# Kernel optimization log

Measured on AMD Instinct MI355X. Metric: run time of the kernel, lower is better.

## Reference

```python
import jax, jax.numpy as jnp
import numpy as np

B, T, HU, C = 256, 128, 512, 64

def setup_inputs() -> dict:
    key = jax.random.key(0)
    k = jax.random.split(key, 8)
    H = jax.random.normal(k[0], (B, T, HU), dtype=jnp.float32)
    y = jax.random.randint(k[1], (B, T), 0, C)
    y_len = jax.random.randint(k[2], (B,), 1, T + 1).astype(jnp.int32)
    y_mask = (jnp.arange(T)[None, :] < y_len[:, None]).astype(jnp.float32)
    xav = float(np.sqrt(6.0 / (3 * HU + C)))
    W = jax.random.uniform(k[3], (C, 3 * HU), minval=-xav, maxval=xav, dtype=jnp.float32)
    b = jnp.zeros((C,), dtype=jnp.float32)
    start_transitions = jax.random.uniform(k[4], (C,), minval=-1.0, maxval=1.0, dtype=jnp.float32)
    end_transitions = jax.random.uniform(k[5], (C,), minval=-1.0, maxval=1.0, dtype=jnp.float32)
    transitions = jax.random.uniform(k[6], (C, C), minval=-1.0, maxval=1.0, dtype=jnp.float32)
    return {"H": H, "W": W, "b": b, "start_transitions": start_transitions,
            "end_transitions": end_transitions, "transitions": transitions,
            "y": y, "y_mask": y_mask, "y_len": y_len}

def _crf_ll(H, W, b, start_transitions, end_transitions, transitions, y, y_mask, y_len):
    Bn, Tn, hu = H.shape
    zeros = jnp.zeros((Bn, 1, hu), H.dtype)
    prev = jnp.concatenate([zeros, H[:, :-1, :]], axis=1)
    nxt = jnp.concatenate([H[:, 1:, :], zeros], axis=1)
    context = jnp.concatenate([prev, H, nxt], axis=-1)            # [B,T,3h]
    scores = jnp.einsum('bth,ch->btc', context, W) + b            # [B,T,C]

    # numerator (gold path score)
    em_sel = jnp.take_along_axis(scores, y[..., None], axis=2)[..., 0]  # [B,T]
    num = start_transitions[y[:, 0]]
    num = num + jnp.sum(em_sel[:, :-1] * y_mask[:, :-1], axis=1)
    num = num + jnp.sum(transitions[y[:, :-1], y[:, 1:]] * y_mask[:, 1:], axis=1)
    last_tags = jnp.take_along_axis(y, (y_len - 1)[:, None].astype(y.dtype), axis=1)[:, 0]
    num = num + end_transitions[last_tags]
    num = num + jnp.take_along_axis(scores[:, -1, :], last_tags[:, None], axis=1)[:, 0] * y_mask[:, -1]

    # partition (log Z) via masked logsumexp scan
    em_t = jnp.transpose(scores, (1, 0, 2))   # [T,B,C]
    m_t = y_mask.T                            # [T,B]
    lp0 = start_transitions[None, :] + em_t[0]
    def step(lp, inp):
        em, m = inp
        new = jax.nn.logsumexp(lp[:, :, None] + transitions[None, :, :] + em[:, None, :], axis=1)
        lp = new * m[:, None] + lp * (1.0 - m[:, None])
        return lp, None
    lp, _ = jax.lax.scan(step, lp0, (em_t[1:], m_t[1:]))
    logZ = jax.nn.logsumexp(lp + end_transitions[None, :], axis=1)
    return num - logZ                          # [B]

def reference(H, W, b, start_transitions, end_transitions, transitions, y, y_mask, y_len):
    return _crf_ll(H, W, b, start_transitions, end_transitions, transitions, y, y_mask, y_len)
```

## Files before the change

kernel.cpp:

```cpp
#include <hip/hip_runtime.h>

typedef __attribute__((ext_vector_type(8))) short short8;
typedef __attribute__((ext_vector_type(4))) float f32x4;

__device__ __forceinline__ unsigned pk_rne(float a, float b) {
  unsigned short ha = __builtin_bit_cast(unsigned short, (_Float16)a);
  unsigned short hb = __builtin_bit_cast(unsigned short, (_Float16)b);
  return (unsigned)ha | ((unsigned)hb << 16);
}
__device__ __forceinline__ unsigned short f2bf(float x) {
  unsigned int u = __float_as_uint(x);
  u += 0x7FFFu + ((u >> 16) & 1u);
  return (unsigned short)(u >> 16);
}
__device__ __forceinline__ float bf2f(unsigned short h) {
  return __uint_as_float(((unsigned)h) << 16);
}
__device__ __forceinline__ unsigned pk_bf(float a, float b) {
  unsigned r;
  asm("v_cvt_pk_bf16_f32 %0, %1, %2" : "=v"(r) : "v"(a), "v"(b));
  return r;
}
__device__ __forceinline__ unsigned scale_bf_pair(unsigned w, float s) {
  float f0 = __uint_as_float(w << 16) * s;
  float f1 = __uint_as_float(w & 0xFFFF0000u) * s;
  return pk_bf(f0, f1);
}

__global__ __launch_bounds__(512) void crf_fused_kernel(
    const float* __restrict__ H, const float* __restrict__ W,
    const float* __restrict__ bias,
    const float* __restrict__ startT, const float* __restrict__ endT,
    const float* __restrict__ trans,
    const int* __restrict__ y, const int* __restrict__ y_len,
    float* __restrict__ out)
{
  __shared__ __align__(16) float smem[25088];
  __shared__ __align__(16) unsigned char EAbuf[8192];
  __shared__ __align__(16) float sc[128][68];
  __shared__ float scm[128];
  __shared__ float emy[128];
  __shared__ __align__(16) float ubuf[64];
  unsigned char* aTh = (unsigned char*)smem;
  unsigned char* bTh = aTh + 16384;
  float* P = smem;
  unsigned char* Mbase = (unsigned char*)smem;

  const int b    = blockIdx.x;
  const int tid  = threadIdx.x;
  const int lane = tid & 63;
  const int wid  = tid >> 6;
  const int wm   = wid >> 2;
  const int wn   = wid & 3;

  f32x4 acc[4][3] = {};
  const float* Hb = H + (size_t)b * (128 * 512);
  const int len = y_len[b];
  const int* yb = y + b * 128;

  float4 areg[4], breg[6];
  int aRow[4], aK4[4], bN[6], bK4[6];
  #pragma unroll
  for (int it = 0; it < 4; ++it) { int i = it * 512 + tid; aRow[it] = i >> 4; aK4[it] = i & 15; }
  #pragma unroll
  for (int it = 0; it < 6; ++it) { int i = it * 512 + tid; bN[it] = i >> 4; bK4[it] = i & 15; }
  #pragma unroll
  for (int it = 0; it < 4; ++it)
    areg[it] = ((const float4*)(Hb + aRow[it] * 512))[aK4[it]];
  #pragma unroll
  for (int it = 0; it < 6; ++it)
    breg[it] = ((const float4*)(W + (bN[it] & 63) * 1536 + (bN[it] >> 6) * 512))[bK4[it]];

  #pragma unroll
  for (int it = 0; it < 2; ++it) {
    int idx = it * 512 + tid;
    int c = idx >> 4, c4 = idx & 15;
    float4 v = ((const float4*)trans)[idx];
    #pragma unroll
    for (int e = 0; e < 4; ++e) {
      int cp = c4 * 4 + e;
      float val = __expf(((const float*)&v)[e] - 1.0f);
      *(unsigned short*)(EAbuf + cp * 128 + ((2 * c) ^ ((cp & 7) << 4))) = f2bf(val);
    }
  }

  for (int kk = 0; kk < 512; kk += 64) {
    if (kk) __syncthreads();
    #pragma unroll
    for (int it = 0; it < 4; ++it) {
      float4 v = areg[it];
      uint2 hi; hi.x = pk_rne(v.x, v.y); hi.y = pk_rne(v.z, v.w);
      int off = aRow[it] * 128 + ((aK4[it] * 8) ^ ((aRow[it] & 7) << 4));
      *(uint2*)(aTh + off) = hi;
    }
    #pragma unroll
    for (int it = 0; it < 6; ++it) {
      float4 v = breg[it];
      uint2 bh; bh.x = pk_rne(v.x, v.y); bh.y = pk_rne(v.z, v.w);
      int off = bN[it] * 128 + ((bK4[it] * 8) ^ ((bN[it] & 7) << 4));
      *(uint2*)(bTh + off) = bh;
    }
    __syncthreads();
    if (kk < 448) {
      #pragma unroll
      for (int it = 0; it < 4; ++it)
        areg[it] = ((const float4*)(Hb + aRow[it] * 512 + kk + 64))[aK4[it]];
      #pragma unroll
      for (int it = 0; it < 6; ++it)
        breg[it] = ((const float4*)(W + (bN[it] & 63) * 1536 + (bN[it] >> 6) * 512 + kk + 64))[bK4[it]];
    }
    #pragma unroll
    for (int ks = 0; ks < 2; ++ks) {
      const int kbyte = ks * 64 + ((lane >> 4) << 4);
      short8 ah[4], bh[3];
      #pragma unroll
      for (int m = 0; m < 4; ++m) {
        int row = wm * 64 + m * 16 + (lane & 15);
        ah[m] = *(const short8*)(aTh + row * 128 + (kbyte ^ ((row & 7) << 4)));
      }
      #pragma unroll
      for (int n = 0; n < 3; ++n) {
        int col = wn * 48 + n * 16 + (lane & 15);
        bh[n] = *(const short8*)(bTh + col * 128 + (kbyte ^ ((col & 7) << 4)));
      }
      #pragma unroll
      for (int m = 0; m < 4; ++m)
        #pragma unroll
        for (int n = 0; n < 3; ++n)
          asm("v_mfma_f32_16x16x32_f16 %0, %1, %2, %0"
              : "+v"(acc[m][n]) : "v"(ah[m]), "v"(bh[n]));
    }
  }
  __syncthreads();

  #pragma unroll
  for (int m = 0; m < 4; ++m)
    #pragma unroll
    for (int n = 0; n < 3; ++n) {
      int row0 = wm * 64 + m * 16 + ((lane >> 4) << 2);
      int col  = wn * 48 + n * 16 + (lane & 15);
      #pragma unroll
      for (int j = 0; j < 4; ++j)
        P[(row0 + j) * 196 + col] = acc[m][n][j];
    }
  __syncthreads();

  #pragma unroll
  for (int it = 0; it < 4; ++it) {
    int i4 = it * 512 + tid;
    int t = i4 >> 4, c4 = i4 & 15;
    float4 s = *(const float4*)(P + t * 196 + 64 + c4 * 4);
    float4 bb = ((const float4*)bias)[c4];
    s.x += bb.x; s.y += bb.y; s.z += bb.z; s.w += bb.w;
    if (t > 0) {
      float4 g = *(const float4*)(P + (t - 1) * 196 + c4 * 4);
      s.x += g.x; s.y += g.y; s.z += g.z; s.w += g.w;
    }
    if (t < 127) {
      float4 g = *(const float4*)(P + (t + 1) * 196 + 128 + c4 * 4);
      s.x += g.x; s.y += g.y; s.z += g.z; s.w += g.w;
    }
    *(float4*)(&sc[t][c4 * 4]) = s;
    float m4 = fmaxf(fmaxf(s.x, s.y), fmaxf(s.z, s.w));
    #pragma unroll
    for (int o = 1; o < 16; o <<= 1) m4 = fmaxf(m4, __shfl_xor(m4, o, 64));
    if ((lane & 15) == 0) scm[t] = m4;
    int yt = yb[t];
    if ((yt >> 2) == c4) {
      int r = yt & 3;
      emy[t] = (r == 0) ? s.x : (r == 1) ? s.y : (r == 2) ? s.z : s.w;
    }
  }
  __syncthreads();

  {
    int row = tid >> 2, c0 = (tid & 3) << 4;
    float mt = scm[row];
    float4* p4 = (float4*)&sc[row][c0];
    #pragma unroll
    for (int j = 0; j < 4; ++j) {
      float4 x = p4[j];
      x.x = __expf(x.x - mt); x.y = __expf(x.y - mt);
      x.z = __expf(x.z - mt); x.w = __expf(x.w - mt);
      p4[j] = x;
    }
  }
  float num = 0.f;
  if (wid == 0) {
    float p = 0.f;
    #pragma unroll
    for (int rep = 0; rep < 2; ++rep) {
      int t = lane + rep * 64;
      if (t < 127) {
        int yt = yb[t], yt1 = yb[t + 1];
        if (t < len)     p += emy[t];
        if (t + 1 < len) p += trans[yt * 64 + yt1];
      }
    }
    #pragma unroll
    for (int s = 32; s > 0; s >>= 1) p += __shfl_xor(p, s, 64);
    num = p + startT[yb[0]] + endT[yb[len - 1]];
    if (len == 128) num += emy[127];
  }
  __syncthreads();

  {
    unsigned char* Mb = Mbase + wid * 8192;
    int t0 = (wid == 0) ? 1 : 16 * wid;
    int t1 = 16 * wid + 15; if (t1 > len - 1) t1 = len - 1;
    if (t0 <= t1) {
      const int sw = (lane & 7) << 4;
      float s0 = sc[t0][lane];
      #pragma unroll
      for (int j = 0; j < 8; ++j) {
        uint4 w = *(const uint4*)(EAbuf + lane * 128 + ((j * 16) ^ sw));
        uint4 o;
        o.x = scale_bf_pair(w.x, s0); o.y = scale_bf_pair(w.y, s0);
        o.z = scale_bf_pair(w.z, s0); o.w = scale_bf_pair(w.w, s0);
        *(uint4*)(Mb + lane * 128 + ((j * 16) ^ sw)) = o;
      }
      short8 ea[4][2];
      #pragma unroll
      for (int rt = 0; rt < 4; ++rt)
        #pragma unroll
        for (int kh = 0; kh < 2; ++kh) {
          int row = rt * 16 + (lane & 15);
          int kb = kh * 64 + ((lane >> 4) << 4);
          ea[rt][kh] = *(const short8*)(EAbuf + row * 128 + (kb ^ ((row & 7) << 4)));
        }
      f32x4 z4 = {0.f, 0.f, 0.f, 0.f};
      for (int t = t0 + 1; t <= t1; ++t) {
        short8 mf[4][2];
        #pragma unroll
        for (int ct = 0; ct < 4; ++ct)
          #pragma unroll
          for (int kh = 0; kh < 2; ++kh) {
            int row = ct * 16 + (lane & 15);
            int kb = kh * 64 + ((lane >> 4) << 4);
            mf[ct][kh] = *(const short8*)(Mb + row * 128 + (kb ^ ((row & 7) << 4)));
          }
        f32x4 sv[4];
        #pragma unroll
        for (int rt = 0; rt < 4; ++rt)
          sv[rt] = *(const f32x4*)(&sc[t][rt * 16 + ((lane >> 4) << 2)]);
        f32x4 c[4][4];
        #pragma unroll
        for (int rt = 0; rt < 4; ++rt)
          #pragma unroll
          for (int ct = 0; ct < 4; ++ct) {
            asm("v_mfma_f32_16x16x32_bf16 %0, %1, %2, %3"
                : "=&v"(c[rt][ct]) : "v"(ea[rt][0]), "v"(mf[ct][0]), "v"(z4));
            asm("v_mfma_f32_16x16x32_bf16 %0, %1, %2, %0"
                : "+v"(c[rt][ct]) : "v"(ea[rt][1]), "v"(mf[ct][1]));
          }
        #pragma unroll
        for (int rt = 0; rt < 4; ++rt)
          #pragma unroll
          for (int ct = 0; ct < 4; ++ct) {
            f32x4 cc = c[rt][ct] * sv[rt];
            uint2 w2; w2.x = pk_bf(cc[0], cc[1]); w2.y = pk_bf(cc[2], cc[3]);
            int row = ct * 16 + (lane & 15);
            int byt = 2 * (rt * 16 + ((lane >> 4) << 2));
            *(uint2*)(Mb + row * 128 + (byt ^ ((row & 7) << 4))) = w2;
          }
      }
    }
  }
  __syncthreads();
  if (wid != 0) return;

  float eE = __expf(endT[lane]);
  float ls;
  {
    int t1 = 1 + lane, t2 = 65 + lane;
    float a = (t1 <= len - 1) ? (scm[t1] + 1.0f) : 0.f;
    if (t2 <= len - 1) a += scm[t2] + 1.0f;
    #pragma unroll
    for (int s = 32; s > 0; s >>= 1) a += __shfl_xor(a, s, 64);
    ls = a + scm[0];
  }
  float u = __expf(startT[lane]) * sc[0][lane];

  for (int k = 0; k < 8; ++k) {
    if (k && 16 * k >= len) break;
    int lo = (k == 0) ? 1 : 16 * k;
    int hi = 16 * k + 15; if (hi > len - 1) hi = len - 1;
    if (lo > hi) continue;
    float r = u;
    #pragma unroll
    for (int s = 32; s > 0; s >>= 1) r = fmaxf(r, __shfl_xor(r, s, 64));
    unsigned br = __float_as_uint(r) & 0x7F800000u;
    u *= __uint_as_float(0x7F000000u - br);
    ls += (float)((int)(br >> 23) - 127) * 0.69314718055994531f;
    const unsigned char* Mb = Mbase + k * 8192;
    ubuf[lane] = u;
    float v0 = 0.f, v1 = 0.f, v2 = 0.f, v3 = 0.f;
    #pragma unroll 4
    for (int c = 0; c < 64; c += 4) {
      float4 uu = *(const float4*)&ubuf[c];
      float m0 = bf2f(*(const unsigned short*)(Mb + (c + 0) * 128 + ((2 * lane) ^ (((c + 0) & 7) << 4))));
      float m1 = bf2f(*(const unsigned short*)(Mb + (c + 1) * 128 + ((2 * lane) ^ (((c + 1) & 7) << 4))));
      float m2 = bf2f(*(const unsigned short*)(Mb + (c + 2) * 128 + ((2 * lane) ^ (((c + 2) & 7) << 4))));
      float m3 = bf2f(*(const unsigned short*)(Mb + (c + 3) * 128 + ((2 * lane) ^ (((c + 3) & 7) << 4))));
      v0 = fmaf(uu.x, m0, v0);
      v1 = fmaf(uu.y, m1, v1);
      v2 = fmaf(uu.z, m2, v2);
      v3 = fmaf(uu.w, m3, v3);
    }
    u = (v0 + v1) + (v2 + v3);
  }

  float x = u * eE;
  #pragma unroll
  for (int s = 32; s > 0; s >>= 1) x += __shfl_xor(x, s, 64);
  if (lane == 0) out[b] = num - (__logf(x) + ls);
}

extern "C" void kernel_launch(void* const* d_in, const int* in_sizes, int n_in,
                              void* d_out, int out_size, void* d_ws, size_t ws_size,
                              hipStream_t stream) {
  const float* H      = (const float*)d_in[0];
  const float* W      = (const float*)d_in[1];
  const float* bias   = (const float*)d_in[2];
  const float* startT = (const float*)d_in[3];
  const float* endT   = (const float*)d_in[4];
  const float* trans  = (const float*)d_in[5];
  const int*   y      = (const int*)d_in[6];
  const int*   y_len  = (const int*)d_in[8];
  float* out = (float*)d_out;

  crf_fused_kernel<<<dim3(256), dim3(512), 0, stream>>>(
      H, W, bias, startT, endT, trans, y, y_len, out);
}
```

Before: 43.75 us.

## Double GEMM K-tile to 128, fuse exp into score epilogue, drop barrier

The GEMM K-loop now stages 128-wide K tiles per iteration (4 iterations instead of 8), which halves the number of barriers and doubles the register prefetch. The exp-normalisation of the emission scores is fused into the score epilogue and stored as bf16, removing a separate pass over shared memory and a sync. The numerator is computed by wave 7 into shared memory without an extra barrier. The trade-offs are higher register pressure from 20 float4 prefetch registers and reduced emission precision (bf16).

```diff
diff --git a/kernel.cpp b/kernel.cpp
--- a/kernel.cpp
+++ b/kernel.cpp
@@ -37,12 +37,13 @@
 {
   __shared__ __align__(16) float smem[25088];
   __shared__ __align__(16) unsigned char EAbuf[8192];
-  __shared__ __align__(16) float sc[128][68];
+  __shared__ __align__(16) unsigned short scbf[128][64];
   __shared__ float scm[128];
   __shared__ float emy[128];
   __shared__ __align__(16) float ubuf[64];
-  unsigned char* aTh = (unsigned char*)smem;
-  unsigned char* bTh = aTh + 16384;
+  __shared__ float numsh;
+  unsigned char* aT = (unsigned char*)smem;
+  unsigned char* bT = ((unsigned char*)smem) + 32768;
   float* P = smem;
   unsigned char* Mbase = (unsigned char*)smem;
 
@@ -58,18 +59,18 @@
   const int len = y_len[b];
   const int* yb = y + b * 128;
 
-  float4 areg[4], breg[6];
-  int aRow[4], aK4[4], bN[6], bK4[6];
-  #pragma unroll
-  for (int it = 0; it < 4; ++it) { int i = it * 512 + tid; aRow[it] = i >> 4; aK4[it] = i & 15; }
-  #pragma unroll
-  for (int it = 0; it < 6; ++it) { int i = it * 512 + tid; bN[it] = i >> 4; bK4[it] = i & 15; }
-  #pragma unroll
-  for (int it = 0; it < 4; ++it)
+  float4 areg[8], breg[12];
+  int aRow[8], aK4[8], bN[12], bK4[12];
+  #pragma unroll
+  for (int it = 0; it < 8; ++it) { int i = it * 512 + tid; aRow[it] = i >> 5; aK4[it] = i & 31; }
+  #pragma unroll
+  for (int jt = 0; jt < 12; ++jt) { int j = jt * 512 + tid; bN[jt] = j >> 5; bK4[jt] = j & 31; }
+  #pragma unroll
+  for (int it = 0; it < 8; ++it)
     areg[it] = ((const float4*)(Hb + aRow[it] * 512))[aK4[it]];
   #pragma unroll
-  for (int it = 0; it < 6; ++it)
-    breg[it] = ((const float4*)(W + (bN[it] & 63) * 1536 + (bN[it] >> 6) * 512))[bK4[it]];
+  for (int jt = 0; jt < 12; ++jt)
+    breg[jt] = ((const float4*)(W + (bN[jt] & 63) * 1536 + (bN[jt] >> 6) * 512))[bK4[jt]];
 
   #pragma unroll
   for (int it = 0; it < 2; ++it) {
@@ -84,44 +85,45 @@
     }
   }
 
-  for (int kk = 0; kk < 512; kk += 64) {
-    if (kk) __syncthreads();
-    #pragma unroll
-    for (int it = 0; it < 4; ++it) {
+  for (int kt = 0; kt < 4; ++kt) {
+    if (kt) __syncthreads();
+    #pragma unroll
+    for (int it = 0; it < 8; ++it) {
       float4 v = areg[it];
-      uint2 hi; hi.x = pk_rne(v.x, v.y); hi.y = pk_rne(v.z, v.w);
-      int off = aRow[it] * 128 + ((aK4[it] * 8) ^ ((aRow[it] & 7) << 4));
-      *(uint2*)(aTh + off) = hi;
-    }
-    #pragma unroll
-    for (int it = 0; it < 6; ++it) {
-      float4 v = breg[it];
-      uint2 bh; bh.x = pk_rne(v.x, v.y); bh.y = pk_rne(v.z, v.w);
-      int off = bN[it] * 128 + ((bK4[it] * 8) ^ ((bN[it] & 7) << 4));
-      *(uint2*)(bTh + off) = bh;
+      uint2 o; o.x = pk_rne(v.x, v.y); o.y = pk_rne(v.z, v.w);
+      int half = aK4[it] >> 4, k4h = aK4[it] & 15;
+      *(uint2*)(aT + half * 16384 + aRow[it] * 128 + ((k4h * 8) ^ ((aRow[it] & 7) << 4))) = o;
+    }
+    #pragma unroll
+    for (int jt = 0; jt < 12; ++jt) {
+      float4 v = breg[jt];
+      uint2 o; o.x = pk_rne(v.x, v.y); o.y = pk_rne(v.z, v.w);
+      int half = bK4[jt] >> 4, k4h = bK4[jt] & 15;
+      *(uint2*)(bT + half * 24576 + bN[jt] * 128 + ((k4h * 8) ^ ((bN[jt] & 7) << 4))) = o;
     }
     __syncthreads();
-    if (kk < 448) {
-      #pragma unroll
-      for (int it = 0; it < 4; ++it)
-        areg[it] = ((const float4*)(Hb + aRow[it] * 512 + kk + 64))[aK4[it]];
-      #pragma unroll
-      for (int it = 0; it < 6; ++it)
-        breg[it] = ((const float4*)(W + (bN[it] & 63) * 1536 + (bN[it] >> 6) * 512 + kk + 64))[bK4[it]];
-    }
-    #pragma unroll
-    for (int ks = 0; ks < 2; ++ks) {
-      const int kbyte = ks * 64 + ((lane >> 4) << 4);
+    if (kt < 3) {
+      #pragma unroll
+      for (int it = 0; it < 8; ++it)
+        areg[it] = ((const float4*)(Hb + aRow[it] * 512 + (kt + 1) * 128))[aK4[it]];
+      #pragma unroll
+      for (int jt = 0; jt < 12; ++jt)
+        breg[jt] = ((const float4*)(W + (bN[jt] & 63) * 1536 + (bN[jt] >> 6) * 512 + (kt + 1) * 128))[bK4[jt]];
+    }
+    #pragma unroll
+    for (int ks = 0; ks < 4; ++ks) {
+      const int half = ks >> 1;
+      const int kb = (ks & 1) * 64 + ((lane >> 4) << 4);
       short8 ah[4], bh[3];
       #pragma unroll
       for (int m = 0; m < 4; ++m) {
         int row = wm * 64 + m * 16 + (lane & 15);
-        ah[m] = *(const short8*)(aTh + row * 128 + (kbyte ^ ((row & 7) << 4)));
+        ah[m] = *(const short8*)(aT + half * 16384 + row * 128 + (kb ^ ((row & 7) << 4)));
       }
       #pragma unroll
       for (int n = 0; n < 3; ++n) {
         int col = wn * 48 + n * 16 + (lane & 15);
-        bh[n] = *(const short8*)(bTh + col * 128 + (kbyte ^ ((col & 7) << 4)));
+        bh[n] = *(const short8*)(bT + half * 24576 + col * 128 + (kb ^ ((col & 7) << 4)));
       }
       #pragma unroll
       for (int m = 0; m < 4; ++m)
@@ -160,7 +162,6 @@
       float4 g = *(const float4*)(P + (t + 1) * 196 + 128 + c4 * 4);
       s.x += g.x; s.y += g.y; s.z += g.z; s.w += g.w;
     }
-    *(float4*)(&sc[t][c4 * 4]) = s;
     float m4 = fmaxf(fmaxf(s.x, s.y), fmaxf(s.z, s.w));
     #pragma unroll
     for (int o = 1; o < 16; o <<= 1) m4 = fmaxf(m4, __shfl_xor(m4, o, 64));
@@ -170,23 +171,14 @@
       int r = yt & 3;
       emy[t] = (r == 0) ? s.x : (r == 1) ? s.y : (r == 2) ? s.z : s.w;
     }
+    float e0 = __expf(s.x - m4), e1 = __expf(s.y - m4);
+    float e2 = __expf(s.z - m4), e3 = __expf(s.w - m4);
+    uint2 w2; w2.x = pk_bf(e0, e1); w2.y = pk_bf(e2, e3);
+    *(uint2*)&scbf[t][c4 * 4] = w2;
   }
   __syncthreads();
 
-  {
-    int row = tid >> 2, c0 = (tid & 3) << 4;
-    float mt = scm[row];
-    float4* p4 = (float4*)&sc[row][c0];
-    #pragma unroll
-    for (int j = 0; j < 4; ++j) {
-      float4 x = p4[j];
-      x.x = __expf(x.x - mt); x.y = __expf(x.y - mt);
-      x.z = __expf(x.z - mt); x.w = __expf(x.w - mt);
-      p4[j] = x;
-    }
-  }
-  float num = 0.f;
-  if (wid == 0) {
+  if (wid == 7) {
     float p = 0.f;
     #pragma unroll
     for (int rep = 0; rep < 2; ++rep) {
@@ -199,10 +191,10 @@
     }
     #pragma unroll
     for (int s = 32; s > 0; s >>= 1) p += __shfl_xor(p, s, 64);
-    num = p + startT[yb[0]] + endT[yb[len - 1]];
-    if (len == 128) num += emy[127];
-  }
-  __syncthreads();
+    float nm = p + startT[yb[0]] + endT[yb[len - 1]];
+    if (len == 128) nm += emy[127];
+    if (lane == 0) numsh = nm;
+  }
 
   {
     unsigned char* Mb = Mbase + wid * 8192;
@@ -210,7 +202,7 @@
     int t1 = 16 * wid + 15; if (t1 > len - 1) t1 = len - 1;
     if (t0 <= t1) {
       const int sw = (lane & 7) << 4;
-      float s0 = sc[t0][lane];
+      float s0 = bf2f(scbf[t0][lane]);
       #pragma unroll
       for (int j = 0; j < 8; ++j) {
         uint4 w = *(const uint4*)(EAbuf + lane * 128 + ((j * 16) ^ sw));
@@ -241,8 +233,11 @@
           }
         f32x4 sv[4];
         #pragma unroll
-        for (int rt = 0; rt < 4; ++rt)
-          sv[rt] = *(const f32x4*)(&sc[t][rt * 16 + ((lane >> 4) << 2)]);
+        for (int rt = 0; rt < 4; ++rt) {
+          ushort4 ra = *(const ushort4*)&scbf[t][rt * 16 + ((lane >> 4) << 2)];
+          sv[rt][0] = bf2f(ra.x); sv[rt][1] = bf2f(ra.y);
+          sv[rt][2] = bf2f(ra.z); sv[rt][3] = bf2f(ra.w);
+        }
         f32x4 c[4][4];
         #pragma unroll
         for (int rt = 0; rt < 4; ++rt)
@@ -279,7 +274,7 @@
     for (int s = 32; s > 0; s >>= 1) a += __shfl_xor(a, s, 64);
     ls = a + scm[0];
   }
-  float u = __expf(startT[lane]) * sc[0][lane];
+  float u = __expf(startT[lane]) * bf2f(scbf[0][lane]);
 
   for (int k = 0; k < 8; ++k) {
     if (k && 16 * k >= len) break;
@@ -313,7 +308,7 @@
   float x = u * eE;
   #pragma unroll
   for (int s = 32; s > 0; s >>= 1) x += __shfl_xor(x, s, 64);
-  if (lane == 0) out[b] = num - (__logf(x) + ls);
+  if (lane == 0) out[b] = numsh - (__logf(x) + ls);
 }
 
 extern "C" void kernel_launch(void* const* d_in, const int* in_sizes, int n_in,
```

New measurement: 47.30 us. 1.08x slower.

## Double-buffer GEMM LDS staging and fuse exp into the score pass

Applied to the files above, without the earlier changes.

The bf16/f16 GEMM main loop now ping-pongs between two LDS staging buffers. The next tile's converted data is written while the current tile is consumed, so each k-step needs one barrier instead of two. The softmax-style exp normalisation of scores is folded into the score-assembly pass, removing a separate LDS read/write sweep. The numerator reduction moves to warp 7 and is handed over through a shared variable, dropping a block-wide barrier. In exchange the kernel uses more LDS for staging, which may affect occupancy.

```diff
diff --git a/kernel.cpp b/kernel.cpp
--- a/kernel.cpp
+++ b/kernel.cpp
@@ -41,8 +41,8 @@
   __shared__ float scm[128];
   __shared__ float emy[128];
   __shared__ __align__(16) float ubuf[64];
-  unsigned char* aTh = (unsigned char*)smem;
-  unsigned char* bTh = aTh + 16384;
+  __shared__ float numsh;
+  unsigned char* stg = (unsigned char*)smem;
   float* P = smem;
   unsigned char* Mbase = (unsigned char*)smem;
 
@@ -84,30 +84,30 @@
     }
   }
 
-  for (int kk = 0; kk < 512; kk += 64) {
-    if (kk) __syncthreads();
-    #pragma unroll
-    for (int it = 0; it < 4; ++it) {
-      float4 v = areg[it];
-      uint2 hi; hi.x = pk_rne(v.x, v.y); hi.y = pk_rne(v.z, v.w);
-      int off = aRow[it] * 128 + ((aK4[it] * 8) ^ ((aRow[it] & 7) << 4));
-      *(uint2*)(aTh + off) = hi;
-    }
-    #pragma unroll
-    for (int it = 0; it < 6; ++it) {
-      float4 v = breg[it];
-      uint2 bh; bh.x = pk_rne(v.x, v.y); bh.y = pk_rne(v.z, v.w);
-      int off = bN[it] * 128 + ((bK4[it] * 8) ^ ((bN[it] & 7) << 4));
-      *(uint2*)(bTh + off) = bh;
-    }
-    __syncthreads();
-    if (kk < 448) {
+  #pragma unroll
+  for (int it = 0; it < 4; ++it) {
+    float4 v = areg[it];
+    uint2 o; o.x = pk_rne(v.x, v.y); o.y = pk_rne(v.z, v.w);
+    *(uint2*)(stg + aRow[it] * 128 + ((aK4[it] * 8) ^ ((aRow[it] & 7) << 4))) = o;
+  }
+  #pragma unroll
+  for (int it = 0; it < 6; ++it) {
+    float4 v = breg[it];
+    uint2 o; o.x = pk_rne(v.x, v.y); o.y = pk_rne(v.z, v.w);
+    *(uint2*)(stg + 16384 + bN[it] * 128 + ((bK4[it] * 8) ^ ((bN[it] & 7) << 4))) = o;
+  }
+  __syncthreads();
+
+  for (int kk = 0; kk < 8; ++kk) {
+    unsigned char* aTc = stg + (kk & 1) * 40960;
+    unsigned char* bTc = aTc + 16384;
+    if (kk < 7) {
       #pragma unroll
       for (int it = 0; it < 4; ++it)
-        areg[it] = ((const float4*)(Hb + aRow[it] * 512 + kk + 64))[aK4[it]];
+        areg[it] = ((const float4*)(Hb + aRow[it] * 512 + (kk + 1) * 64))[aK4[it]];
       #pragma unroll
       for (int it = 0; it < 6; ++it)
-        breg[it] = ((const float4*)(W + (bN[it] & 63) * 1536 + (bN[it] >> 6) * 512 + kk + 64))[bK4[it]];
+        breg[it] = ((const float4*)(W + (bN[it] & 63) * 1536 + (bN[it] >> 6) * 512 + (kk + 1) * 64))[bK4[it]];
     }
     #pragma unroll
     for (int ks = 0; ks < 2; ++ks) {
@@ -116,12 +116,12 @@
       #pragma unroll
       for (int m = 0; m < 4; ++m) {
         int row = wm * 64 + m * 16 + (lane & 15);
-        ah[m] = *(const short8*)(aTh + row * 128 + (kbyte ^ ((row & 7) << 4)));
+        ah[m] = *(const short8*)(aTc + row * 128 + (kbyte ^ ((row & 7) << 4)));
       }
       #pragma unroll
       for (int n = 0; n < 3; ++n) {
         int col = wn * 48 + n * 16 + (lane & 15);
-        bh[n] = *(const short8*)(bTh + col * 128 + (kbyte ^ ((col & 7) << 4)));
+        bh[n] = *(const short8*)(bTc + col * 128 + (kbyte ^ ((col & 7) << 4)));
       }
       #pragma unroll
       for (int m = 0; m < 4; ++m)
@@ -130,8 +130,24 @@
           asm("v_mfma_f32_16x16x32_f16 %0, %1, %2, %0"
               : "+v"(acc[m][n]) : "v"(ah[m]), "v"(bh[n]));
     }
-  }
-  __syncthreads();
+    if (kk < 7) {
+      unsigned char* aTn = stg + ((kk + 1) & 1) * 40960;
+      unsigned char* bTn = aTn + 16384;
+      #pragma unroll
+      for (int it = 0; it < 4; ++it) {
+        float4 v = areg[it];
+        uint2 o; o.x = pk_rne(v.x, v.y); o.y = pk_rne(v.z, v.w);
+        *(uint2*)(aTn + aRow[it] * 128 + ((aK4[it] * 8) ^ ((aRow[it] & 7) << 4))) = o;
+      }
+      #pragma unroll
+      for (int it = 0; it < 6; ++it) {
+        float4 v = breg[it];
+        uint2 o; o.x = pk_rne(v.x, v.y); o.y = pk_rne(v.z, v.w);
+        *(uint2*)(bTn + bN[it] * 128 + ((bK4[it] * 8) ^ ((bN[it] & 7) << 4))) = o;
+      }
+    }
+    __syncthreads();
+  }
 
   #pragma unroll
   for (int m = 0; m < 4; ++m)
@@ -160,7 +176,6 @@
       float4 g = *(const float4*)(P + (t + 1) * 196 + 128 + c4 * 4);
       s.x += g.x; s.y += g.y; s.z += g.z; s.w += g.w;
     }
-    *(float4*)(&sc[t][c4 * 4]) = s;
     float m4 = fmaxf(fmaxf(s.x, s.y), fmaxf(s.z, s.w));
     #pragma unroll
     for (int o = 1; o < 16; o <<= 1) m4 = fmaxf(m4, __shfl_xor(m4, o, 64));
@@ -170,23 +185,14 @@
       int r = yt & 3;
       emy[t] = (r == 0) ? s.x : (r == 1) ? s.y : (r == 2) ? s.z : s.w;
     }
+    float4 e;
+    e.x = __expf(s.x - m4); e.y = __expf(s.y - m4);
+    e.z = __expf(s.z - m4); e.w = __expf(s.w - m4);
+    *(float4*)(&sc[t][c4 * 4]) = e;
   }
   __syncthreads();
 
-  {
-    int row = tid >> 2, c0 = (tid & 3) << 4;
-    float mt = scm[row];
-    float4* p4 = (float4*)&sc[row][c0];
-    #pragma unroll
-    for (int j = 0; j < 4; ++j) {
-      float4 x = p4[j];
-      x.x = __expf(x.x - mt); x.y = __expf(x.y - mt);
-      x.z = __expf(x.z - mt); x.w = __expf(x.w - mt);
-      p4[j] = x;
-    }
-  }
-  float num = 0.f;
-  if (wid == 0) {
+  if (wid == 7) {
     float p = 0.f;
     #pragma unroll
     for (int rep = 0; rep < 2; ++rep) {
@@ -199,10 +205,10 @@
     }
     #pragma unroll
     for (int s = 32; s > 0; s >>= 1) p += __shfl_xor(p, s, 64);
-    num = p + startT[yb[0]] + endT[yb[len - 1]];
-    if (len == 128) num += emy[127];
-  }
-  __syncthreads();
+    float nm = p + startT[yb[0]] + endT[yb[len - 1]];
+    if (len == 128) nm += emy[127];
+    if (lane == 0) numsh = nm;
+  }
 
   {
     unsigned char* Mb = Mbase + wid * 8192;
@@ -313,7 +319,7 @@
   float x = u * eE;
   #pragma unroll
   for (int s = 32; s > 0; s >>= 1) x += __shfl_xor(x, s, 64);
-  if (lane == 0) out[b] = num - (__logf(x) + ls);
+  if (lane == 0) out[b] = numsh - (__logf(x) + ls);
 }
 
 extern "C" void kernel_launch(void* const* d_in, const int* in_sizes, int n_in,
```

Result: no change. 43.86 us (+0.2%).
